# Optimization experiments

Hardware: AMD Instinct MI355X
Metric: run time of the kernel (lower is better)

## Reference

```python
import jax, jax.numpy as jnp
import numpy as np

GAMMA = 1.0  # init arg gamma


def setup_inputs() -> dict:
    key = jax.random.key(0)
    ks = jax.random.split(key, 7)
    Bn, C, C_, H = 8, 256, 32, 64
    sc = 1.0 / np.sqrt(C)
    return {
        "x_activation": jax.random.normal(ks[0], (Bn, C, H, H), dtype=jnp.float32),
        "f_w": jax.random.normal(ks[1], (C_, C), dtype=jnp.float32) * sc,
        "f_b": jnp.zeros((C_,), dtype=jnp.float32),
        "g_w": jax.random.normal(ks[2], (C_, C), dtype=jnp.float32) * sc,
        "g_b": jnp.zeros((C_,), dtype=jnp.float32),
        "h_w": jax.random.normal(ks[3], (C, C), dtype=jnp.float32) * sc,
        "h_b": jnp.zeros((C,), dtype=jnp.float32),
    }


def reference(x_activation, f_w, f_b, g_w, g_b, h_w, h_b):
    Bn, C, H, W = x_activation.shape
    N = H * W
    xf = x_activation.reshape(Bn, C, N)  # [B, C, N]
    # 1x1 convs are per-pixel linear maps over channels
    f = jnp.einsum('oc,bcn->bon', f_w, xf) + f_b[:, None]  # [B, C_, N]
    g = jnp.einsum('oc,bcn->bon', g_w, xf) + g_b[:, None]  # [B, C_, N]
    h = jnp.einsum('oc,bcn->bon', h_w, xf) + h_b[:, None]  # [B, C, N]
    # S[b, i, j] = sum_c f[b, c, i] * g[b, c, j]  (f^T @ g), shape [B, N, N]
    S = jnp.einsum('bci,bcj->bij', f, g)
    # NOTE: original uses Softmax(dim=1) -> normalize over the i (query/f) axis
    B = jax.nn.softmax(S, axis=1)
    # O (post-transpose) [b, c, i] = sum_j B[b, i, j] * h[b, c, j]
    O = jnp.einsum('bij,bcj->bci', B, h).reshape(Bn, C, H, W)
    return GAMMA * O + x_activation
```

## Files before the change

### kernel.cpp

```cpp
#include <hip/hip_runtime.h>
#include <hip/hip_fp16.h>
#include <cmath>


#define BN 8
#define CC 256
#define CQ 32
#define NN 4096

typedef _Float16 half8 __attribute__((ext_vector_type(8)));
typedef _Float16 half4v __attribute__((ext_vector_type(4)));
typedef float f32x4 __attribute__((ext_vector_type(4)));

static __device__ __forceinline__ float fexp2(float x) {
    return __builtin_amdgcn_exp2f(x);
}

#define LOG2E 1.44269504f
#define SHIFT2 28.8539008f

__global__ __launch_bounds__(256) void cvtw_kernel(
    const float* __restrict__ fw, const float* __restrict__ gw,
    const float* __restrict__ hw, __half* __restrict__ wf16)
{
    int i = blockIdx.x * 256 + threadIdx.x;
    float v;
    if (i < 8192)       v = fw[i];
    else if (i < 16384) v = gw[i - 8192];
    else                v = hw[i - 16384];
    wf16[i] = __float2half(v);
}

__global__ __launch_bounds__(256) void tp_proj_kernel(
    const float* __restrict__ x, const __half* __restrict__ wf16,
    const float* __restrict__ fb, const float* __restrict__ gb,
    const float* __restrict__ hb,
    __half* __restrict__ ft, __half* __restrict__ gt, __half* __restrict__ hm)
{
    const int tid = threadIdx.x;
    const int w = tid >> 6, lane = tid & 63, col = lane & 15, q = lane >> 4;
    const int gid = blockIdx.x;
    const int b  = gid & 7;
    const int n0 = (gid >> 3) * 64;

    __shared__ float  T[64 * 65];
    __shared__ __half XT[64 * 256];

    const int u  = tid >> 4;
    const int n4 = (tid & 15) * 4;
    const int nn = w * 16 + (lane >> 2);
    const int cc = (lane & 3) * 16;
    const int sA = 8 * (nn & 7);
    for (int c4 = 0; c4 < 4; ++c4) {
        const int c0 = c4 * 64;
        const float* xb = x + ((size_t)b * CC + c0) * NN + n0;
#pragma unroll
        for (int r = 0; r < 4; ++r) {
            int c = r * 16 + u;
            f32x4 v = __builtin_nontemporal_load((const f32x4*)(xb + (size_t)c * NN + n4));
            T[c * 65 + n4 + 0] = v.x;
            T[c * 65 + n4 + 1] = v.y;
            T[c * 65 + n4 + 2] = v.z;
            T[c * 65 + n4 + 3] = v.w;
        }
        __syncthreads();
        half8 o0, o1;
#pragma unroll
        for (int k = 0; k < 8; ++k) {
            o0[k] = (_Float16)T[(cc + k) * 65 + nn];
            o1[k] = (_Float16)T[(cc + 8 + k) * 65 + nn];
        }
        *(half8*)(void*)(&XT[nn * 256 + ((c0 + cc) ^ sA)])     = o0;
        *(half8*)(void*)(&XT[nn * 256 + ((c0 + cc + 8) ^ sA)]) = o1;
        __syncthreads();
    }

    const f32x4 zero = {0.f, 0.f, 0.f, 0.f};
    const int sw = 8 * (col & 7);

    {
        const __half* fw16 = wf16;
        const __half* gw16 = wf16 + 8192;
        f32x4 acc[4];
#pragma unroll
        for (int mt = 0; mt < 4; ++mt) acc[mt] = zero;
        const int pixl = 16 * w + col;
#pragma unroll
        for (int ks = 0; ks < 8; ++ks) {
            half8 bf = *(const half8*)(const void*)(
                &XT[pixl * 256 + ((ks * 32 + q * 8) ^ sw)]);
#pragma unroll
            for (int mt = 0; mt < 4; ++mt) {
                const __half* wp = (mt < 2) ? (fw16 + (16 * mt + col) * CC)
                                            : (gw16 + (16 * (mt - 2) + col) * CC);
                half8 af = *(const half8*)(const void*)(wp + ks * 32 + q * 8);
                acc[mt] = __builtin_amdgcn_mfma_f32_16x16x32_f16(af, bf, acc[mt], 0, 0, 0);
            }
        }
        const int pix = n0 + pixl;
#pragma unroll
        for (int mt = 0; mt < 4; ++mt) {
            const int mtl = mt & 1;
            const float* bsel = (mt < 2) ? fb : gb;
            __half* dsel = (mt < 2) ? ft : gt;
            half4v hv;
#pragma unroll
            for (int r = 0; r < 4; ++r)
                hv[r] = (_Float16)(acc[mt][r] + bsel[16 * mtl + 4 * q + r]);
            *(half4v*)(void*)(dsel + ((size_t)b * NN + pix) * CQ + 16 * mtl + 4 * q) = hv;
        }
    }

    {
        const __half* hw16 = wf16 + 16384;
        f32x4 acc[4][4];
#pragma unroll
        for (int mt = 0; mt < 4; ++mt)
#pragma unroll
            for (int ci = 0; ci < 4; ++ci) acc[mt][ci] = zero;
#pragma unroll
        for (int ks = 0; ks < 8; ++ks) {
            half8 af[4], bf[4];
#pragma unroll
            for (int mt = 0; mt < 4; ++mt)
                af[mt] = *(const half8*)(const void*)(
                    &XT[(16 * mt + col) * 256 + ((ks * 32 + q * 8) ^ sw)]);
#pragma unroll
            for (int ci = 0; ci < 4; ++ci)
                bf[ci] = *(const half8*)(const void*)(
                    hw16 + (size_t)(16 * (4 * w + ci) + col) * CC + ks * 32 + q * 8);
#pragma unroll
            for (int mt = 0; mt < 4; ++mt)
#pragma unroll
                for (int ci = 0; ci < 4; ++ci)
                    acc[mt][ci] = __builtin_amdgcn_mfma_f32_16x16x32_f16(
                        af[mt], bf[ci], acc[mt][ci], 0, 0, 0);
        }
#pragma unroll
        for (int ci = 0; ci < 4; ++ci) {
            const int c = 16 * (4 * w + ci) + col;
            const float bias = hb[c];
#pragma unroll
            for (int mt = 0; mt < 4; ++mt) {
                half4v hv;
#pragma unroll
                for (int r = 0; r < 4; ++r)
                    hv[r] = (_Float16)(acc[mt][ci][r] + bias);
                *(half4v*)(void*)(hm + ((size_t)b * CC + c) * NN + n0 + 16 * mt + 4 * q) = hv;
            }
        }
    }
}

__global__ __launch_bounds__(256) void pass1_kernel(
    const __half* __restrict__ ft, const __half* __restrict__ gt,
    float* __restrict__ shl)
{
    const int tid = threadIdx.x;
    const int w = tid >> 6, lane = tid & 63, col = lane & 15, q = lane >> 4;
    const int gid = blockIdx.x;
    const int b = gid & 7;
    const int jg = (gid >> 3) * 64 + 16 * w + col;

    const __half* fbase = ft + (size_t)b * NN * CQ;
    half8 gfrag = *(const half8*)(const void*)(gt + ((size_t)b * NN + jg) * CQ + q * 8);

    float a0 = 0.f, a1 = 0.f, a2 = 0.f, a3 = 0.f;
    const f32x4 zero = {0.f, 0.f, 0.f, 0.f};

    half8 a0v = *(const half8*)(const void*)(fbase + (size_t)col * CQ + q * 8);
    half8 a1v = *(const half8*)(const void*)(fbase + (size_t)(16 + col) * CQ + q * 8);
    for (int i0 = 0; i0 < NN; i0 += 32) {
        int i_n = (i0 + 32) & (NN - 1);
        half8 a2v = *(const half8*)(const void*)(fbase + (size_t)(i_n + col) * CQ + q * 8);
        half8 a3v = *(const half8*)(const void*)(fbase + (size_t)(i_n + 16 + col) * CQ + q * 8);
        f32x4 d0 = __builtin_amdgcn_mfma_f32_16x16x32_f16(a0v, gfrag, zero, 0, 0, 0);
        f32x4 d1 = __builtin_amdgcn_mfma_f32_16x16x32_f16(a1v, gfrag, zero, 0, 0, 0);
        a0 += fexp2(fmaf(d0[0], LOG2E, -SHIFT2)) + fexp2(fmaf(d1[0], LOG2E, -SHIFT2));
        a1 += fexp2(fmaf(d0[1], LOG2E, -SHIFT2)) + fexp2(fmaf(d1[1], LOG2E, -SHIFT2));
        a2 += fexp2(fmaf(d0[2], LOG2E, -SHIFT2)) + fexp2(fmaf(d1[2], LOG2E, -SHIFT2));
        a3 += fexp2(fmaf(d0[3], LOG2E, -SHIFT2)) + fexp2(fmaf(d1[3], LOG2E, -SHIFT2));
        a0v = a2v;
        a1v = a3v;
    }
    float l = (a0 + a1) + (a2 + a3);
    l += __shfl_xor(l, 16);
    l += __shfl_xor(l, 32);
    if (q == 0)
        shl[(size_t)b * NN + jg] = -__log2f(l) - SHIFT2;
}

__global__ __launch_bounds__(256, 2) void pass2_kernel(
    const float* __restrict__ x,
    const __half* __restrict__ ft, const __half* __restrict__ gt,
    const __half* __restrict__ hm, const float* __restrict__ shl,
    float* __restrict__ out)
{
    const int tid = threadIdx.x;
    const int w = tid >> 6, lane = tid & 63, col = lane & 15, q = lane >> 4;
    const int gid = blockIdx.x;
    const int b  = gid & 7;
    const int i0 = (gid >> 3) * 64;
    const int cb = 64 * w;

    __shared__ __half P[2][64 * 64];

    const __half* gbase = gt + (size_t)b * NN * CQ;
    const __half* hbase = hm + (size_t)b * CC * NN;
    const float*  lb    = shl + (size_t)b * NN;

    half8 ffr[4];
#pragma unroll
    for (int it = 0; it < 4; ++it)
        ffr[it] = *(const half8*)(const void*)(ft + ((size_t)b * NN + i0 + 16 * it + col) * CQ + q * 8);

    f32x4 acc[4][4];
#pragma unroll
    for (int ms = 0; ms < 4; ++ms)
#pragma unroll
        for (int ns = 0; ns < 4; ++ns)
            acc[ms][ns] = (f32x4){0.f, 0.f, 0.f, 0.f};

    const f32x4 zero = {0.f, 0.f, 0.f, 0.f};
    const int jml = 16 * w + 4 * q;
    const int sw  = 8 * (col & 7);

    half8 gfr = *(const half8*)(const void*)(gbase + (size_t)(16 * w + col) * CQ + q * 8);
    f32x4 sl  = *(const f32x4*)(lb + jml);

    int buf = 0;
    for (int j0 = 0; j0 < NN; j0 += 64, buf ^= 1) {
        half8 hv[4][2];
#pragma unroll
        for (int ns = 0; ns < 4; ++ns)
#pragma unroll
            for (int ks = 0; ks < 2; ++ks)
                hv[ns][ks] = *(const half8*)(const void*)(
                    hbase + (size_t)(cb + 16 * ns + col) * NN + j0 + ks * 32 + q * 8);

        f32x4 d[4];
#pragma unroll
        for (int it = 0; it < 4; ++it)
            d[it] = __builtin_amdgcn_mfma_f32_16x16x32_f16(gfr, ffr[it], zero, 0, 0, 0);

        const int jn = (j0 + 64) & (NN - 1);
        half8 gfr_n = *(const half8*)(const void*)(gbase + (size_t)(jn + 16 * w + col) * CQ + q * 8);
        f32x4 sl_n  = *(const f32x4*)(lb + jn + jml);

        __half* Pb = &P[buf][0];
#pragma unroll
        for (int it = 0; it < 4; ++it) {
            half4v pv;
            pv[0] = (_Float16)fexp2(fmaf(d[it][0], LOG2E, sl[0]));
            pv[1] = (_Float16)fexp2(fmaf(d[it][1], LOG2E, sl[1]));
            pv[2] = (_Float16)fexp2(fmaf(d[it][2], LOG2E, sl[2]));
            pv[3] = (_Float16)fexp2(fmaf(d[it][3], LOG2E, sl[3]));
            *(half4v*)(void*)(Pb + (16 * it + col) * 64 + (jml ^ sw)) = pv;
        }
        __syncthreads();

#pragma unroll
        for (int ks = 0; ks < 2; ++ks) {
            half8 af[4];
#pragma unroll
            for (int ms = 0; ms < 4; ++ms)
                af[ms] = *(const half8*)(const void*)(
                    Pb + (16 * ms + col) * 64 + ((ks * 32 + q * 8) ^ sw));
#pragma unroll
            for (int ms = 0; ms < 4; ++ms)
#pragma unroll
                for (int ns = 0; ns < 4; ++ns)
                    acc[ms][ns] = __builtin_amdgcn_mfma_f32_16x16x32_f16(
                        af[ms], hv[ns][ks], acc[ms][ns], 0, 0, 0);
        }
        gfr = gfr_n;
        sl  = sl_n;
    }

    const float* xb = x + (size_t)b * CC * NN;
    float* ob = out + (size_t)b * CC * NN;
#pragma unroll
    for (int ms = 0; ms < 4; ++ms) {
#pragma unroll
        for (int ns = 0; ns < 4; ++ns) {
            int c  = cb + 16 * ns + col;
            int ii = i0 + 16 * ms + 4 * q;
            size_t off = (size_t)c * NN + ii;
            f32x4 xv = __builtin_nontemporal_load((const f32x4*)(xb + off));
            f32x4 ov;
            ov.x = acc[ms][ns][0] + xv.x;
            ov.y = acc[ms][ns][1] + xv.y;
            ov.z = acc[ms][ns][2] + xv.z;
            ov.w = acc[ms][ns][3] + xv.w;
            __builtin_nontemporal_store(ov, (f32x4*)(ob + off));
        }
    }
}

extern "C" void kernel_launch(void* const* d_in, const int* in_sizes, int n_in,
                              void* d_out, int out_size, void* d_ws, size_t ws_size,
                              hipStream_t stream)
{
    const float* x  = (const float*)d_in[0];
    const float* fw = (const float*)d_in[1];
    const float* fb = (const float*)d_in[2];
    const float* gw = (const float*)d_in[3];
    const float* gb = (const float*)d_in[4];
    const float* hw = (const float*)d_in[5];
    const float* hb = (const float*)d_in[6];
    float* out = (float*)d_out;

    char* ws = (char*)d_ws;
    __half* wf = (__half*)(ws);
    __half* ft = (__half*)(ws + (size_t)262144);
    __half* gt = (__half*)(ws + (size_t)2359296);
    __half* hm = (__half*)(ws + (size_t)4456448);
    float*  lv = (float*) (ws + (size_t)21233664);

    cvtw_kernel<<<dim3(320), dim3(256), 0, stream>>>(fw, gw, hw, wf);
    tp_proj_kernel<<<dim3(512), dim3(256), 0, stream>>>(x, wf, fb, gb, hb, ft, gt, hm);
    pass1_kernel<<<dim3(512), dim3(256), 0, stream>>>(ft, gt, lv);
    pass2_kernel<<<dim3(512), dim3(256), 0, stream>>>(x, ft, gt, hm, lv, out);
}
```

Baseline: 294.1 us.

## Split softmax denominator pass over query chunks and batch x loads in projection

The column-sum pass is split across four query-range chunks, launching four times as many blocks that each write partial sums, followed by a small kernel that combines the partials and takes the log. This raises parallelism for the exp-heavy reduction on a GPU with many CUs, at the cost of an extra launch and a partial-sum buffer round trip. Separately, the projection kernel now issues all 16 x loads up front into registers before the transpose loop, increasing memory-level parallelism at the cost of register pressure.

```diff
diff --git a/kernel.cpp b/kernel.cpp
--- a/kernel.cpp
+++ b/kernel.cpp
@@ -51,17 +51,26 @@
     const int nn = w * 16 + (lane >> 2);
     const int cc = (lane & 3) * 16;
     const int sA = 8 * (nn & 7);
+
+    f32x4 vx[4][4];
+    const float* xb = x + (size_t)b * CC * NN + n0;
+#pragma unroll
+    for (int c4 = 0; c4 < 4; ++c4)
+#pragma unroll
+        for (int r = 0; r < 4; ++r)
+            vx[c4][r] = __builtin_nontemporal_load(
+                (const f32x4*)(xb + (size_t)(c4 * 64 + r * 16 + u) * NN + n4));
+
+#pragma unroll
     for (int c4 = 0; c4 < 4; ++c4) {
         const int c0 = c4 * 64;
-        const float* xb = x + ((size_t)b * CC + c0) * NN + n0;
 #pragma unroll
         for (int r = 0; r < 4; ++r) {
             int c = r * 16 + u;
-            f32x4 v = __builtin_nontemporal_load((const f32x4*)(xb + (size_t)c * NN + n4));
-            T[c * 65 + n4 + 0] = v.x;
-            T[c * 65 + n4 + 1] = v.y;
-            T[c * 65 + n4 + 2] = v.z;
-            T[c * 65 + n4 + 3] = v.w;
+            T[c * 65 + n4 + 0] = vx[c4][r].x;
+            T[c * 65 + n4 + 1] = vx[c4][r].y;
+            T[c * 65 + n4 + 2] = vx[c4][r].z;
+            T[c * 65 + n4 + 3] = vx[c4][r].w;
         }
         __syncthreads();
         half8 o0, o1;
@@ -152,15 +161,18 @@
     }
 }
 
-__global__ __launch_bounds__(256) void pass1_kernel(
+__global__ __launch_bounds__(256) void pass1a_kernel(
     const __half* __restrict__ ft, const __half* __restrict__ gt,
-    float* __restrict__ shl)
+    float* __restrict__ lpart)
 {
     const int tid = threadIdx.x;
     const int w = tid >> 6, lane = tid & 63, col = lane & 15, q = lane >> 4;
     const int gid = blockIdx.x;
-    const int b = gid & 7;
-    const int jg = (gid >> 3) * 64 + 16 * w + col;
+    const int b  = gid & 7;
+    const int jt = (gid >> 3) & 63;
+    const int iq = gid >> 9;
+    const int jg = jt * 64 + 16 * w + col;
+    const int ibase = iq * 1024;
 
     const __half* fbase = ft + (size_t)b * NN * CQ;
     half8 gfrag = *(const half8*)(const void*)(gt + ((size_t)b * NN + jg) * CQ + q * 8);
@@ -168,10 +180,10 @@
     float a0 = 0.f, a1 = 0.f, a2 = 0.f, a3 = 0.f;
     const f32x4 zero = {0.f, 0.f, 0.f, 0.f};
 
-    half8 a0v = *(const half8*)(const void*)(fbase + (size_t)col * CQ + q * 8);
-    half8 a1v = *(const half8*)(const void*)(fbase + (size_t)(16 + col) * CQ + q * 8);
-    for (int i0 = 0; i0 < NN; i0 += 32) {
-        int i_n = (i0 + 32) & (NN - 1);
+    half8 a0v = *(const half8*)(const void*)(fbase + (size_t)(ibase + col) * CQ + q * 8);
+    half8 a1v = *(const half8*)(const void*)(fbase + (size_t)(ibase + 16 + col) * CQ + q * 8);
+    for (int t = 0; t < 32; ++t) {
+        int i_n = ibase + ((t + 1) & 31) * 32;
         half8 a2v = *(const half8*)(const void*)(fbase + (size_t)(i_n + col) * CQ + q * 8);
         half8 a3v = *(const half8*)(const void*)(fbase + (size_t)(i_n + 16 + col) * CQ + q * 8);
         f32x4 d0 = __builtin_amdgcn_mfma_f32_16x16x32_f16(a0v, gfrag, zero, 0, 0, 0);
@@ -187,7 +199,23 @@
     l += __shfl_xor(l, 16);
     l += __shfl_xor(l, 32);
     if (q == 0)
-        shl[(size_t)b * NN + jg] = -__log2f(l) - SHIFT2;
+        lpart[((size_t)iq * BN + b) * NN + jg] = l;
+}
+
+__global__ __launch_bounds__(256) void pass1b_kernel(
+    const float* __restrict__ lpart, float* __restrict__ shl)
+{
+    const int i4 = (blockIdx.x * 256 + threadIdx.x) * 4;
+    f32x4 s0 = *(const f32x4*)(lpart + i4);
+    f32x4 s1 = *(const f32x4*)(lpart + 1 * BN * NN + i4);
+    f32x4 s2 = *(const f32x4*)(lpart + 2 * BN * NN + i4);
+    f32x4 s3 = *(const f32x4*)(lpart + 3 * BN * NN + i4);
+    f32x4 o;
+    o.x = -__log2f((s0.x + s1.x) + (s2.x + s3.x)) - SHIFT2;
+    o.y = -__log2f((s0.y + s1.y) + (s2.y + s3.y)) - SHIFT2;
+    o.z = -__log2f((s0.z + s1.z) + (s2.z + s3.z)) - SHIFT2;
+    o.w = -__log2f((s0.w + s1.w) + (s2.w + s3.w)) - SHIFT2;
+    *(f32x4*)(shl + i4) = o;
 }
 
 __global__ __launch_bounds__(256, 2) void pass2_kernel(
@@ -316,9 +344,11 @@
     __half* gt = (__half*)(ws + (size_t)2359296);
     __half* hm = (__half*)(ws + (size_t)4456448);
     float*  lv = (float*) (ws + (size_t)21233664);
+    float*  lp = (float*) (ws + (size_t)21364736);
 
     cvtw_kernel<<<dim3(320), dim3(256), 0, stream>>>(fw, gw, hw, wf);
     tp_proj_kernel<<<dim3(512), dim3(256), 0, stream>>>(x, wf, fb, gb, hb, ft, gt, hm);
-    pass1_kernel<<<dim3(512), dim3(256), 0, stream>>>(ft, gt, lv);
+    pass1a_kernel<<<dim3(2048), dim3(256), 0, stream>>>(ft, gt, lp);
+    pass1b_kernel<<<dim3(32), dim3(256), 0, stream>>>(lp, lv);
     pass2_kernel<<<dim3(512), dim3(256), 0, stream>>>(x, ft, gt, hm, lv, out);
 }
```

Result: no change. 289.8 us (-1.4%).
